# Performance work log

Hardware: AMD Instinct MI355X
Metric: run time of the kernel (lower is better)

The kernel has to match this reference:

```python
import jax, jax.numpy as jnp
import numpy as np

HIDDEN = 4096
N_HEADS = 32
N_KV_HEADS = 2
HEAD_DIM = 128          # hidden // n_heads
ROT_DIM = HEAD_DIM // 2  # partial rotary (ChatGLM style)
ROPE_THETA = 10000.0
Q_SIZE = N_HEADS * HEAD_DIM
KV_SIZE = N_KV_HEADS * HEAD_DIM
SCALE = HEAD_DIM ** -0.5
T = 2048


def setup_inputs() -> dict:
    key = jax.random.key(0)
    k1, k2, k3, k4 = jax.random.split(key, 4)
    hidden_states = jax.random.normal(k1, (T, HIDDEN), dtype=jnp.float32)
    positions = jnp.arange(T, dtype=jnp.int64) if jax.config.jax_enable_x64 else jnp.arange(T, dtype=jnp.int32)
    w_qkv = jax.random.normal(k2, (Q_SIZE + 2 * KV_SIZE, HIDDEN), dtype=jnp.float32) * 0.02
    b_qkv = jax.random.normal(k3, (Q_SIZE + 2 * KV_SIZE,), dtype=jnp.float32) * 0.02
    w_dense = jax.random.normal(k4, (HIDDEN, Q_SIZE), dtype=jnp.float32) * 0.02
    return {"hidden_states": hidden_states, "positions": positions,
            "w_qkv": w_qkv, "b_qkv": b_qkv, "w_dense": w_dense}


def _apply_rope(x, positions):
    # x: [T, H, HEAD_DIM]; interleaved (is_neox_style=False) partial rotary on first ROT_DIM dims
    half = ROT_DIM // 2
    inv_freq = 1.0 / (ROPE_THETA ** (jnp.arange(0, half, dtype=jnp.float32) * 2.0 / ROT_DIM))
    freqs = positions.astype(jnp.float32)[:, None] * inv_freq[None, :]   # [T, half]
    cos = jnp.cos(freqs)[:, None, :]  # [T, 1, half]
    sin = jnp.sin(freqs)[:, None, :]
    x_rot = x[..., :ROT_DIM]
    x_pass = x[..., ROT_DIM:]
    x1 = x_rot[..., 0::2]
    x2 = x_rot[..., 1::2]
    o1 = x1 * cos - x2 * sin
    o2 = x2 * cos + x1 * sin
    rot = jnp.stack([o1, o2], axis=-1).reshape(x_rot.shape)  # re-interleave
    return jnp.concatenate([rot, x_pass], axis=-1)


def reference(hidden_states, positions, w_qkv, b_qkv, w_dense):
    # QKV projection (bias from add_qkv_bias=True)
    qkv = hidden_states @ w_qkv.T + b_qkv                     # [T, 4608]
    q = qkv[:, :Q_SIZE].reshape(T, N_HEADS, HEAD_DIM)
    k = qkv[:, Q_SIZE:Q_SIZE + KV_SIZE].reshape(T, N_KV_HEADS, HEAD_DIM)
    v = qkv[:, Q_SIZE + KV_SIZE:].reshape(T, N_KV_HEADS, HEAD_DIM)

    q = _apply_rope(q, positions)
    k = _apply_rope(k, positions)

    # GQA: expand 2 kv heads -> 32 q heads (each kv head serves 16 q heads)
    rep = N_HEADS // N_KV_HEADS
    k = jnp.repeat(k, rep, axis=1)                            # [T, 32, 128]
    v = jnp.repeat(v, rep, axis=1)

    # Causal scaled dot-product attention
    scores = jnp.einsum('thd,shd->hts', q, k) * SCALE         # [H, T, T]
    causal = positions[:, None] >= positions[None, :]          # [T, T]
    scores = jnp.where(causal[None, :, :], scores, jnp.finfo(scores.dtype).min)
    probs = jax.nn.softmax(scores, axis=-1)
    attn = jnp.einsum('hts,shd->thd', probs, v).reshape(T, Q_SIZE)

    # Output projection (no bias: add_bias_linear=False)
    return attn @ w_dense.T
```

## Files before the change

kernel.cpp:

```cpp
#include <hip/hip_runtime.h>
#include <cstdint>
#include <math.h>

typedef __bf16 bf16;
typedef __bf16 bf16x8 __attribute__((ext_vector_type(8)));
typedef __bf16 bf16x4 __attribute__((ext_vector_type(4)));
typedef float f32x4 __attribute__((ext_vector_type(4)));

#define T_SEQ 2048
#define HID   4096
#define NQH   32
#define NKVH  2
#define HD    128
#define NQKV  4608
#define ATT_SCALE 0.08838834764831845f

__device__ __forceinline__ void load_lds16(const void* g, void* l) {
    auto gp = (const __attribute__((address_space(1))) unsigned int*)(uintptr_t)g;
    auto lp = (__attribute__((address_space(3))) unsigned int*)(unsigned int)(uintptr_t)l;
    __builtin_amdgcn_global_load_lds(gp, lp, 16, 0, 0);
}

__device__ __forceinline__ f32x4 mfma16(bf16x8 a, bf16x8 b, f32x4 c) {
    return __builtin_amdgcn_mfma_f32_16x16x32_bf16(a, b, c, 0, 0, 0);
}

__global__ void cvt_f32_bf16_kernel(const float* __restrict__ x, bf16* __restrict__ y) {
    size_t i = ((size_t)blockIdx.x * 256 + threadIdx.x) * 8;
    float4 a = *(const float4*)(x + i);
    float4 b = *(const float4*)(x + i + 4);
    bf16x8 o;
    o[0] = (bf16)a.x; o[1] = (bf16)a.y; o[2] = (bf16)a.z; o[3] = (bf16)a.w;
    o[4] = (bf16)b.x; o[5] = (bf16)b.y; o[6] = (bf16)b.z; o[7] = (bf16)b.w;
    *(bf16x8*)(y + i) = o;
}

template <int OUT_BF16, int HAS_BIAS>
__global__ __launch_bounds__(256) void gemm_bt(const bf16* __restrict__ A,
                                               const bf16* __restrict__ B,
                                               const float* __restrict__ bias,
                                               void* __restrict__ Cout,
                                               int M, int N, int K) {
    __shared__ __align__(16) char sA[16384];
    __shared__ __align__(16) char sB[16384];
    const int tid = threadIdx.x;
    const int wid = tid >> 6, l = tid & 63, l4 = l >> 4, l16 = l & 15;
    const int wm = wid >> 1, wn = wid & 1;
    const int bm = blockIdx.x * 128, bn = blockIdx.y * 128;

    f32x4 acc[4][4] = {};

    for (int k0 = 0; k0 < K; k0 += 64) {
        __syncthreads();
#pragma unroll
        for (int c4 = 0; c4 < 4; ++c4) {
            int ch = c4 * 256 + tid;
            int row = ch >> 3, cch = ch & 7;
            int scc = cch ^ (row & 7);
            load_lds16(A + (size_t)(bm + row) * K + k0 + scc * 8,
                       sA + c4 * 4096 + wid * 1024);
        }
#pragma unroll
        for (int c4 = 0; c4 < 4; ++c4) {
            int ch = c4 * 256 + tid;
            int row = ch >> 3, cch = ch & 7;
            int scc = cch ^ (row & 7);
            load_lds16(B + (size_t)(bn + row) * K + k0 + scc * 8,
                       sB + c4 * 4096 + wid * 1024);
        }
        __syncthreads();
#pragma unroll
        for (int ks = 0; ks < 2; ++ks) {
            bf16x8 af[4], bfr[4];
#pragma unroll
            for (int mi = 0; mi < 4; ++mi) {
                int row = wm * 64 + mi * 16 + l16;
                af[mi] = *(const bf16x8*)(sA + row * 128 + ((ks * 64 + l4 * 16) ^ ((row & 7) << 4)));
            }
#pragma unroll
            for (int ni = 0; ni < 4; ++ni) {
                int row = wn * 64 + ni * 16 + l16;
                bfr[ni] = *(const bf16x8*)(sB + row * 128 + ((ks * 64 + l4 * 16) ^ ((row & 7) << 4)));
            }
#pragma unroll
            for (int mi = 0; mi < 4; ++mi)
#pragma unroll
                for (int ni = 0; ni < 4; ++ni)
                    acc[mi][ni] = mfma16(af[mi], bfr[ni], acc[mi][ni]);
        }
    }

#pragma unroll
    for (int mi = 0; mi < 4; ++mi)
#pragma unroll
        for (int ni = 0; ni < 4; ++ni) {
            const int col = bn + wn * 64 + ni * 16 + l16;
            float bv = HAS_BIAS ? bias[col] : 0.0f;
#pragma unroll
            for (int r = 0; r < 4; ++r) {
                const int row = bm + wm * 64 + mi * 16 + l4 * 4 + r;
                float val = acc[mi][ni][r] + bv;
                if (OUT_BF16)
                    ((bf16*)Cout)[(size_t)row * N + col] = (bf16)val;
                else
                    ((float*)Cout)[(size_t)row * N + col] = val;
            }
        }
}

__global__ void rope_qk_kernel(const bf16* __restrict__ qkv,
                               bf16* __restrict__ qheads, bf16* __restrict__ kheads) {
    const int t = blockIdx.x;
    const int g = blockIdx.y;
    const int sub = threadIdx.x >> 6;
    const int l = threadIdx.x & 63;
    const bf16* src;
    bf16* dst;
    if (g < 8) {
        int hh = g * 4 + sub;
        src = qkv + (size_t)t * NQKV + hh * HD;
        dst = qheads + ((size_t)hh * T_SEQ + t) * HD;
    } else {
        if (sub >= 2) return;
        src = qkv + (size_t)t * NQKV + HID + sub * HD;
        dst = kheads + ((size_t)sub * T_SEQ + t) * HD;
    }
    if (l < 32) {
        const int i = l;
        float x1 = (float)src[2 * i], x2 = (float)src[2 * i + 1];
        float fr = (float)t * exp2f((float)i * (-13.287712379549449f / 32.0f));
        float sn = sinf(fr), cs = cosf(fr);
        dst[2 * i] = (bf16)(x1 * cs - x2 * sn);
        dst[2 * i + 1] = (bf16)(x2 * cs + x1 * sn);
    } else {
        const int j = l - 32;
        dst[64 + 2 * j] = src[64 + 2 * j];
        dst[64 + 2 * j + 1] = src[64 + 2 * j + 1];
    }
}

__global__ void v_trans_kernel(const bf16* __restrict__ qkv, bf16* __restrict__ vt) {
    const int c = threadIdx.x;
    const int kvh = c >> 7, d = c & 127;
    const int t0 = blockIdx.x * 8;
#pragma unroll
    for (int i = 0; i < 8; ++i) {
        int t = t0 + i;
        vt[((size_t)kvh * HD + d) * T_SEQ + t] = qkv[(size_t)t * NQKV + 4352 + c];
    }
}

__global__ __launch_bounds__(256, 2) void attn_fwd_kernel(const bf16* __restrict__ qh,
                                                          const bf16* __restrict__ kh,
                                                          const bf16* __restrict__ vt,
                                                          bf16* __restrict__ attnb) {
    __shared__ __align__(16) char sK[2][16384];
    __shared__ __align__(16) char sV[2][16384];
    __shared__ __align__(16) char sP[4][4096];
    const int tid = threadIdx.x;
    const int wid = tid >> 6, l = tid & 63, l4 = l >> 4, l16 = l & 15;
    const int b = blockIdx.x;
    const int qb = 15 - (b >> 5);
    const int h = b & 31, kvh = h >> 4;
    const int qbase = qb * 128 + wid * 32;

    auto stageKV = [&](int buf, int kt) {
#pragma unroll
        for (int c4 = 0; c4 < 4; ++c4) {
            int ch = c4 * 256 + tid;
            int row = ch >> 4, cc = ch & 15;
            load_lds16(kh + ((size_t)kvh * T_SEQ + kt * 64 + row) * HD + (cc ^ (row & 7)) * 8,
                       sK[buf] + c4 * 4096 + wid * 1024);
        }
#pragma unroll
        for (int c4 = 0; c4 < 4; ++c4) {
            int ch = c4 * 256 + tid;
            int row = ch >> 3, cc = ch & 7;
            load_lds16(vt + ((size_t)kvh * HD + row) * T_SEQ + kt * 64 + (cc ^ (row & 7)) * 8,
                       sV[buf] + c4 * 4096 + wid * 1024);
        }
    };

    bf16x8 qf[2][4];
#pragma unroll
    for (int rg = 0; rg < 2; ++rg) {
        const bf16* qp = qh + ((size_t)h * T_SEQ + qbase + rg * 16 + l16) * HD + l4 * 8;
#pragma unroll
        for (int f = 0; f < 4; ++f) qf[rg][f] = *(const bf16x8*)(qp + f * 32);
    }
    f32x4 o[2][8] = {};
    float mr[2][4], lr[2][4];
#pragma unroll
    for (int rg = 0; rg < 2; ++rg)
#pragma unroll
        for (int r = 0; r < 4; ++r) { mr[rg][r] = -INFINITY; lr[rg][r] = 0.f; }

    const int nt = 2 * qb + 2;
    stageKV(0, 0);
    __syncthreads();
    int cur = 0;
    for (int kt = 0; kt < nt; ++kt) {
        if (kt + 1 < nt) stageKV(cur ^ 1, kt + 1);

        const bool active = (kt * 64) <= (qbase + 31);
        if (active) {
            f32x4 s[2][4] = {};
#pragma unroll
            for (int ct = 0; ct < 4; ++ct)
#pragma unroll
                for (int ks = 0; ks < 4; ++ks) {
                    int row = ct * 16 + l16;
                    bf16x8 kf = *(const bf16x8*)(sK[cur] + row * 256 + ((ks * 64 + l4 * 16) ^ ((row & 7) << 4)));
                    s[0][ct] = mfma16(qf[0][ks], kf, s[0][ct]);
                    s[1][ct] = mfma16(qf[1][ks], kf, s[1][ct]);
                }

            const bool diag = (kt * 64 + 63 > qbase);
            float sv[2][4][4];
#pragma unroll
            for (int rg = 0; rg < 2; ++rg)
#pragma unroll
                for (int ct = 0; ct < 4; ++ct)
#pragma unroll
                    for (int r = 0; r < 4; ++r) {
                        float x = s[rg][ct][r] * ATT_SCALE;
                        if (diag && (kt * 64 + ct * 16 + l16) > (qbase + rg * 16 + l4 * 4 + r)) x = -INFINITY;
                        sv[rg][ct][r] = x;
                    }

            float pmx[2][4];
            bool ok = true;
#pragma unroll
            for (int rg = 0; rg < 2; ++rg)
#pragma unroll
                for (int r = 0; r < 4; ++r) {
                    pmx[rg][r] = fmaxf(fmaxf(sv[rg][0][r], sv[rg][1][r]), fmaxf(sv[rg][2][r], sv[rg][3][r]));
                    ok = ok && (pmx[rg][r] <= mr[rg][r] + 8.0f);
                }
            if (!__all(ok)) {
#pragma unroll
                for (int rg = 0; rg < 2; ++rg)
#pragma unroll
                    for (int r = 0; r < 4; ++r) {
                        float mx = pmx[rg][r];
                        mx = fmaxf(mx, __shfl_xor(mx, 1));
                        mx = fmaxf(mx, __shfl_xor(mx, 2));
                        mx = fmaxf(mx, __shfl_xor(mx, 4));
                        mx = fmaxf(mx, __shfl_xor(mx, 8));
                        if (mx > mr[rg][r]) {
                            float al = __expf(mr[rg][r] - mx);
                            mr[rg][r] = mx;
                            lr[rg][r] *= al;
#pragma unroll
                            for (int n2 = 0; n2 < 8; ++n2) o[rg][n2][r] *= al;
                        }
                    }
            }
#pragma unroll
            for (int rg = 0; rg < 2; ++rg)
#pragma unroll
                for (int r = 0; r < 4; ++r) {
                    float ps = 0.f;
                    const int prow = rg * 16 + l4 * 4 + r;
#pragma unroll
                    for (int ct = 0; ct < 4; ++ct) {
                        float p = __expf(sv[rg][ct][r] - mr[rg][r]);
                        ps += p;
                        *(bf16*)(sP[wid] + prow * 128 + (((ct * 16 + l16) * 2) ^ ((prow & 7) << 4))) = (bf16)p;
                    }
                    lr[rg][r] += ps;
                }

#pragma unroll
            for (int ks = 0; ks < 2; ++ks) {
                bf16x8 pa0 = *(const bf16x8*)(sP[wid] + l16 * 128 + ((ks * 64 + l4 * 16) ^ ((l16 & 7) << 4)));
                bf16x8 pa1 = *(const bf16x8*)(sP[wid] + (16 + l16) * 128 + ((ks * 64 + l4 * 16) ^ ((l16 & 7) << 4)));
#pragma unroll
                for (int n2 = 0; n2 < 8; ++n2) {
                    int vrow = n2 * 16 + l16;
                    bf16x8 vf = *(const bf16x8*)(sV[cur] + vrow * 128 + ((ks * 64 + l4 * 16) ^ ((vrow & 7) << 4)));
                    o[0][n2] = mfma16(pa0, vf, o[0][n2]);
                    o[1][n2] = mfma16(pa1, vf, o[1][n2]);
                }
            }
        }
        __syncthreads();
        cur ^= 1;
    }

    float inv[2][4];
#pragma unroll
    for (int rg = 0; rg < 2; ++rg)
#pragma unroll
        for (int r = 0; r < 4; ++r) {
            float s2 = lr[rg][r];
            s2 += __shfl_xor(s2, 1);
            s2 += __shfl_xor(s2, 2);
            s2 += __shfl_xor(s2, 4);
            s2 += __shfl_xor(s2, 8);
            inv[rg][r] = 1.0f / s2;
        }
#pragma unroll
    for (int rg = 0; rg < 2; ++rg)
#pragma unroll
        for (int n2 = 0; n2 < 8; ++n2)
#pragma unroll
            for (int r = 0; r < 4; ++r) {
                int row = qb * 128 + wid * 32 + rg * 16 + l4 * 4 + r;
                int col = h * HD + n2 * 16 + l16;
                attnb[(size_t)row * HID + col] = (bf16)(o[rg][n2][r] * inv[rg][r]);
            }
}

extern "C" void kernel_launch(void* const* d_in, const int* in_sizes, int n_in,
                              void* d_out, int out_size, void* d_ws, size_t ws_size,
                              hipStream_t stream) {
    const float* hs = (const float*)d_in[0];
    const float* wqkv = (const float*)d_in[2];
    const float* bqkv = (const float*)d_in[3];
    const float* wdense = (const float*)d_in[4];
    float* out = (float*)d_out;

    char* ws = (char*)d_ws;
    bf16* wqkvb   = (bf16*)(ws + 0);
    bf16* hb      = (bf16*)(ws + 37748736);
    bf16* qkvb    = (bf16*)(ws + 54525952);
    bf16* qhp     = (bf16*)(ws + 0);
    bf16* khp     = (bf16*)(ws + 16777216);
    bf16* vtp     = (bf16*)(ws + 17825792);
    bf16* wdenseb = (bf16*)(ws + 18874368);
    bf16* attnb   = (bf16*)(ws + 54525952);
    (void)in_sizes; (void)n_in; (void)out_size; (void)ws_size;

    cvt_f32_bf16_kernel<<<(T_SEQ * HID) / 2048, 256, 0, stream>>>(hs, hb);
    cvt_f32_bf16_kernel<<<(NQKV * HID) / 2048, 256, 0, stream>>>(wqkv, wqkvb);

    dim3 g1(T_SEQ / 128, NQKV / 128);
    gemm_bt<1, 1><<<g1, 256, 0, stream>>>(hb, wqkvb, bqkv, (void*)qkvb, T_SEQ, NQKV, HID);

    cvt_f32_bf16_kernel<<<(HID * HID) / 2048, 256, 0, stream>>>(wdense, wdenseb);

    rope_qk_kernel<<<dim3(T_SEQ, 9), 256, 0, stream>>>(qkvb, qhp, khp);
    v_trans_kernel<<<T_SEQ / 8, 256, 0, stream>>>(qkvb, vtp);

    attn_fwd_kernel<<<512, 256, 0, stream>>>(qhp, khp, vtp, attnb);

    dim3 g2(T_SEQ / 128, HID / 128);
    gemm_bt<0, 0><<<g2, 256, 0, stream>>>(attnb, wdenseb, nullptr, (void*)out, T_SEQ, HID, HID);
}
```

Measured before the change: 353.2 us.

## Restructure attention KV pipeline with explicit vmcnt waits and single V buffer

Attention now stages V for the current tile and K for the next tile at the start of each iteration. It uses manual s_waitcnt vmcnt counts and raw barriers so the QK^T and softmax phase overlaps the V load, and waits for V only before the PV matmul. V goes from double to single buffered, and launch bounds drop to one block per SIMD. Separately, the V transpose kernel writes 8-element vectors along T instead of scalar scattered stores. The hand-counted vmcnt values are fragile and assume an exact count of outstanding loads, and the lower occupancy hint may reduce latency hiding.

```diff
diff --git a/kernel.cpp b/kernel.cpp
--- a/kernel.cpp
+++ b/kernel.cpp
@@ -14,6 +14,8 @@
 #define HD    128
 #define NQKV  4608
 #define ATT_SCALE 0.08838834764831845f
+
+#define VMCNT(n) asm volatile("s_waitcnt vmcnt(" #n ")" ::: "memory")
 
 __device__ __forceinline__ void load_lds16(const void* g, void* l) {
     auto gp = (const __attribute__((address_space(1))) unsigned int*)(uintptr_t)g;
@@ -140,22 +142,28 @@
 }
 
 __global__ void v_trans_kernel(const bf16* __restrict__ qkv, bf16* __restrict__ vt) {
-    const int c = threadIdx.x;
-    const int kvh = c >> 7, d = c & 127;
-    const int t0 = blockIdx.x * 8;
-#pragma unroll
-    for (int i = 0; i < 8; ++i) {
-        int t = t0 + i;
-        vt[((size_t)kvh * HD + d) * T_SEQ + t] = qkv[(size_t)t * NQKV + 4352 + c];
-    }
-}
-
-__global__ __launch_bounds__(256, 2) void attn_fwd_kernel(const bf16* __restrict__ qh,
+    const int t0 = blockIdx.x * 64;
+    const int kvh = blockIdx.y;
+    const int tid = threadIdx.x;
+#pragma unroll
+    for (int it = 0; it < 4; ++it) {
+        int ch = it * 256 + tid;
+        int d = ch >> 3, tc = ch & 7;
+        int t = t0 + tc * 8;
+        const bf16* src = qkv + (size_t)t * NQKV + 4352 + kvh * HD + d;
+        bf16x8 v;
+#pragma unroll
+        for (int i = 0; i < 8; ++i) v[i] = src[(size_t)i * NQKV];
+        *(bf16x8*)(vt + ((size_t)kvh * HD + d) * T_SEQ + t) = v;
+    }
+}
+
+__global__ __launch_bounds__(256, 1) void attn_fwd_kernel(const bf16* __restrict__ qh,
                                                           const bf16* __restrict__ kh,
                                                           const bf16* __restrict__ vt,
                                                           bf16* __restrict__ attnb) {
     __shared__ __align__(16) char sK[2][16384];
-    __shared__ __align__(16) char sV[2][16384];
+    __shared__ __align__(16) char sV[16384];
     __shared__ __align__(16) char sP[4][4096];
     const int tid = threadIdx.x;
     const int wid = tid >> 6, l = tid & 63, l4 = l >> 4, l16 = l & 15;
@@ -164,7 +172,7 @@
     const int h = b & 31, kvh = h >> 4;
     const int qbase = qb * 128 + wid * 32;
 
-    auto stageKV = [&](int buf, int kt) {
+    auto stageK = [&](int buf, int kt) {
 #pragma unroll
         for (int c4 = 0; c4 < 4; ++c4) {
             int ch = c4 * 256 + tid;
@@ -172,12 +180,14 @@
             load_lds16(kh + ((size_t)kvh * T_SEQ + kt * 64 + row) * HD + (cc ^ (row & 7)) * 8,
                        sK[buf] + c4 * 4096 + wid * 1024);
         }
+    };
+    auto stageV = [&](int kt) {
 #pragma unroll
         for (int c4 = 0; c4 < 4; ++c4) {
             int ch = c4 * 256 + tid;
             int row = ch >> 3, cc = ch & 7;
             load_lds16(vt + ((size_t)kvh * HD + row) * T_SEQ + kt * 64 + (cc ^ (row & 7)) * 8,
-                       sV[buf] + c4 * 4096 + wid * 1024);
+                       sV + c4 * 4096 + wid * 1024);
         }
     };
 
@@ -188,6 +198,9 @@
 #pragma unroll
         for (int f = 0; f < 4; ++f) qf[rg][f] = *(const bf16x8*)(qp + f * 32);
     }
+    VMCNT(0);
+    stageK(0, 0);
+
     f32x4 o[2][8] = {};
     float mr[2][4], lr[2][4];
 #pragma unroll
@@ -196,11 +209,16 @@
         for (int r = 0; r < 4; ++r) { mr[rg][r] = -INFINITY; lr[rg][r] = 0.f; }
 
     const int nt = 2 * qb + 2;
-    stageKV(0, 0);
-    __syncthreads();
     int cur = 0;
     for (int kt = 0; kt < nt; ++kt) {
-        if (kt + 1 < nt) stageKV(cur ^ 1, kt + 1);
+        const bool havenext = (kt + 1 < nt);
+        __builtin_amdgcn_s_barrier();
+        __builtin_amdgcn_sched_barrier(0);
+        stageV(kt);
+        if (havenext) stageK(cur ^ 1, kt + 1);
+        if (havenext) { VMCNT(16); } else { VMCNT(8); }
+        __builtin_amdgcn_s_barrier();
+        __builtin_amdgcn_sched_barrier(0);
 
         const bool active = (kt * 64) <= (qbase + 31);
         if (active) {
@@ -270,7 +288,13 @@
                     }
                     lr[rg][r] += ps;
                 }
-
+        }
+
+        if (havenext) { VMCNT(8); } else { VMCNT(0); }
+        __builtin_amdgcn_s_barrier();
+        __builtin_amdgcn_sched_barrier(0);
+
+        if (active) {
 #pragma unroll
             for (int ks = 0; ks < 2; ++ks) {
                 bf16x8 pa0 = *(const bf16x8*)(sP[wid] + l16 * 128 + ((ks * 64 + l4 * 16) ^ ((l16 & 7) << 4)));
@@ -278,13 +302,12 @@
 #pragma unroll
                 for (int n2 = 0; n2 < 8; ++n2) {
                     int vrow = n2 * 16 + l16;
-                    bf16x8 vf = *(const bf16x8*)(sV[cur] + vrow * 128 + ((ks * 64 + l4 * 16) ^ ((vrow & 7) << 4)));
+                    bf16x8 vf = *(const bf16x8*)(sV + vrow * 128 + ((ks * 64 + l4 * 16) ^ ((vrow & 7) << 4)));
                     o[0][n2] = mfma16(pa0, vf, o[0][n2]);
                     o[1][n2] = mfma16(pa1, vf, o[1][n2]);
                 }
             }
         }
-        __syncthreads();
         cur ^= 1;
     }
 
@@ -341,7 +364,7 @@
     cvt_f32_bf16_kernel<<<(HID * HID) / 2048, 256, 0, stream>>>(wdense, wdenseb);
 
     rope_qk_kernel<<<dim3(T_SEQ, 9), 256, 0, stream>>>(qkvb, qhp, khp);
-    v_trans_kernel<<<T_SEQ / 8, 256, 0, stream>>>(qkvb, vtp);
+    v_trans_kernel<<<dim3(T_SEQ / 64, NKVH), 256, 0, stream>>>(qkvb, vtp);
 
     attn_fwd_kernel<<<512, 256, 0, stream>>>(qhp, khp, vtp, attnb);
 
```

After: 341.1 us. -3.4%, faster.
